# Kernel optimization log

Measured on AMD Instinct MI355X. Metric: run time of the kernel, lower is better.

The kernel has to match this reference:

```python
import jax, jax.numpy as jnp
import numpy as np

B, D, L, K = 262144, 64, 4, 8
BOUND = 3.0
MIN_BW = 1e-3   # min bin width
MIN_BH = 1e-3   # min bin height
MIN_D = 1e-3    # min derivative
MIN_LAM = 0.025 # min lambda
EPS = 1e-6


def _knots(lengths, lo, hi):
    # lengths: (D, K) normalized bin fractions -> (bin lengths (D,K), knot positions (D,K+1))
    knots = jnp.cumsum(lengths, axis=-1)
    knots = jnp.pad(knots, ((0, 0), (1, 0)))
    knots = (hi - lo) * knots + lo
    knots = knots.at[..., 0].set(lo)
    knots = knots.at[..., -1].set(hi)
    return knots[..., 1:] - knots[..., :-1], knots


def _gather(p, idx):
    # p: (D, K'), idx: (B, D) -> (B, D): per-dimension bin-parameter gather
    return p[jnp.arange(p.shape[0])[None, :], idx]


def spline_layer(x, uw, uh, ud, ul):
    # x: (B, D); uw/uh/ul: (D, K); ud: (D, K-1). Linear-order monotonic rational spline (pyro).
    w = jax.nn.softmax(uw, axis=-1)
    h = jax.nn.softmax(uh, axis=-1)
    d = jax.nn.softplus(ud)
    lam = jax.nn.sigmoid(ul)

    num_bins = w.shape[-1]
    left, right = -BOUND, BOUND
    inside = (x >= left) & (x <= right)
    xc = jnp.clip(x, left, right)  # identity applied outside; clamp keeps inside-branch math finite

    w = MIN_BW + (1.0 - MIN_BW * num_bins) * w
    h = MIN_BH + (1.0 - MIN_BH * num_bins) * h
    d = MIN_D + d
    widths, cumw = _knots(w, left, right)
    heights, cumh = _knots(h, left, right)
    d = jnp.pad(d, ((0, 0), (1, 1)), constant_values=1.0)  # boundary derivatives fixed to 1
    lam = (1.0 - 2.0 * MIN_LAM) * lam + MIN_LAM

    # data-dependent bin search (searchsorted via comparison-sum, as in pyro)
    bin_idx = jnp.sum(xc[..., None] >= (cumw + EPS)[None], axis=-1) - 1  # (B, D)
    bin_idx = jnp.clip(bin_idx, 0, num_bins - 1)

    iw = _gather(widths, bin_idx)
    icw = _gather(cumw, bin_idx)
    ich = _gather(cumh, bin_idx)
    idelta = _gather(heights / widths, bin_idx)
    id0 = _gather(d[:, :-1], bin_idx)
    id1 = _gather(d[:, 1:], bin_idx)
    ih = _gather(heights, bin_idx)
    il = _gather(lam, bin_idx)

    wa = 1.0
    wb = jnp.sqrt(id0 / id1) * wa
    wc = (il * wa * id0 + (1.0 - il) * wb * id1) / idelta
    ya = ich
    yb = ih + ich
    yc = ((1.0 - il) * wa * ya + il * wb * yb) / ((1.0 - il) * wa + il * wb)

    theta = (xc - icw) / iw
    lower = theta <= il
    num = jnp.where(lower, wa * ya * (il - theta) + wc * yc * theta,
                    wc * yc * (1.0 - theta) + wb * yb * (theta - il))
    den = jnp.where(lower, wa * (il - theta) + wc * theta,
                    wc * (1.0 - theta) + wb * (theta - il))
    out = num / den
    dnum = jnp.where(lower, wa * wc * il * (yc - ya), wb * wc * (1.0 - il) * (yb - yc)) / iw
    lad = jnp.log(dnum) - 2.0 * jnp.log(jnp.abs(den))

    out = jnp.where(inside, out, x)
    lad = jnp.where(inside, lad, 0.0)
    return out, jnp.sum(lad, axis=1)


def setup_inputs() -> dict:
    key = jax.random.key(0)
    k0, k1, k2, k3, k4 = jax.random.split(key, 5)
    return {
        "x": jax.random.normal(k0, (B, D), dtype=jnp.float32),
        "uw": jax.random.normal(k1, (L, D, K), dtype=jnp.float32),
        "uh": jax.random.normal(k2, (L, D, K), dtype=jnp.float32),
        "ud": jax.random.normal(k3, (L, D, K - 1), dtype=jnp.float32),
        "ul": jax.random.uniform(k4, (L, D, K), dtype=jnp.float32),
    }


def reference(x, uw, uh, ud, ul):
    def step(carry, params):
        xi, ld = carry
        pw, ph, pd, pl = params
        xi, l = spline_layer(xi, pw, ph, pd, pl)
        return (xi, ld + l), None
    init = (x, jnp.zeros(x.shape[0], x.dtype))
    (x, log_det), _ = jax.lax.scan(step, init, (uw, uh, ud, ul))
    return x, log_det
```

## Files before the change

kernel.cpp:

```cpp
#include <hip/hip_runtime.h>


#define BATCH 262144
#define DIM   64
#define NLAY  4
#define NK    8

#define OFF_KN0 0
#define OFF_KN1 2048
#define OFF_CRS 4096
#define OFF_CF0 4544

__global__ void nf_pre(const float* __restrict__ uw, const float* __restrict__ uh,
                       const float* __restrict__ ud, const float* __restrict__ ul,
                       float* __restrict__ F) {
  __shared__ double Lb[NLAY][17], Ly[NLAY][17], LM[NLAY][16][4], Ld[NLAY][16];
  __shared__ double sx[64], Fb[65];
  int d = blockIdx.x;
  int t = threadIdx.x;

  if (t < 32) {
    int l = t >> 3, k = t & 7;
    const float* pw  = uw + (l*DIM + d)*NK;
    const float* ph  = uh + (l*DIM + d)*NK;
    const float* pdv = ud + (l*DIM + d)*(NK-1);
    const float* pl  = ul + (l*DIM + d)*NK;

    float ev[NK];
    float mw = pw[0];
    for (int j = 1; j < NK; ++j) mw = fmaxf(mw, pw[j]);
    float sw = 0.f;
    for (int j = 0; j < NK; ++j) { ev[j] = expf(pw[j] - mw); sw += ev[j]; }
    float invw = 1.f / sw;
    float cwe = 0.f, cwi = 0.f;
    for (int j = 0; j <= k; ++j) {
      float vj = 1e-3f + (1.f - 1e-3f * (float)NK) * (ev[j] * invw);
      cwe = cwi; cwi += vj;
    }
    float kwL = (k == 0) ? -3.f : 6.f * cwe - 3.f;
    float kwR = (k == 7) ?  3.f : 6.f * cwi - 3.f;
    float wwk = kwR - kwL;

    float mh = ph[0];
    for (int j = 1; j < NK; ++j) mh = fmaxf(mh, ph[j]);
    float sh = 0.f;
    for (int j = 0; j < NK; ++j) { ev[j] = expf(ph[j] - mh); sh += ev[j]; }
    float invh = 1.f / sh;
    float che = 0.f, chi = 0.f;
    for (int j = 0; j <= k; ++j) {
      float vj = 1e-3f + (1.f - 1e-3f * (float)NK) * (ev[j] * invh);
      che = chi; chi += vj;
    }
    float khL = (k == 0) ? -3.f : 6.f * che - 3.f;
    float khR = (k == 7) ?  3.f : 6.f * chi - 3.f;
    float hhk = khR - khL;

    float dvk, dvk1;
    if (k == 0) dvk = 1.f;
    else { float u = pdv[k-1]; dvk  = 1e-3f + (fmaxf(u,0.f) + log1pf(expf(-fabsf(u)))); }
    if (k == 7) dvk1 = 1.f;
    else { float u = pdv[k];   dvk1 = 1e-3f + (fmaxf(u,0.f) + log1pf(expf(-fabsf(u)))); }
    float sg = 1.f / (1.f + expf(-pl[k]));
    float lmk = 0.95f * sg + 0.025f;

    float delta = hhk / wwk;
    float wbf = sqrtf(dvk / dvk1);
    float wcf = (lmk*dvk + (1.f-lmk)*wbf*dvk1) / delta;
    float yaf = khL, ybf = hhk + khL;
    float ycf = ((1.f-lmk)*yaf + lmk*wbf*ybf) / ((1.f-lmk) + lmk*wbf);

    if (k == 0) {
      Lb[l][0] = -3.0; Lb[l][16] = 3.0;
      Ly[l][0] = -3.0; Ly[l][16] = 3.0;
    }
    if (k) Lb[l][2*k] = (double)(kwL + 1.0e-6f);
    Lb[l][2*k+1] = (double)kwL + (double)lmk*(double)wwk;
    Ly[l][2*k]   = (double)yaf;
    Ly[l][2*k+1] = (double)ycf;

    double icw = (double)kwL, iw = (double)wwk, il = (double)lmk;
    double wb = wbf, wc = wcf, ya = yaf, yb = ybf, yc = ycf;
    double n0 = ya*il, n1 = wc*yc - ya, d0 = il, d1 = wc - 1.0;
    double A = n1, Bv = n0*iw - n1*icw, C = d1, Dv = d0*iw - d1*icw;
    LM[l][2*k][0]=A; LM[l][2*k][1]=Bv; LM[l][2*k][2]=C; LM[l][2*k][3]=Dv;
    Ld[l][2*k] = log2(A*Dv - Bv*C);
    n0 = wc*yc - il*wb*yb; n1 = wb*yb - wc*yc; d0 = wc - il*wb; d1 = wb - wc;
    A = n1; Bv = n0*iw - n1*icw; C = d1; Dv = d0*iw - d1*icw;
    LM[l][2*k+1][0]=A; LM[l][2*k+1][1]=Bv; LM[l][2*k+1][2]=C; LM[l][2*k+1][3]=Dv;
    Ld[l][2*k+1] = log2(A*Dv - Bv*C);
  }
  __syncthreads();

  if (t < 60) {
    int lp  = t / 15;
    int mth = t % 15 + 1;
    double x = Lb[lp][mth];
    for (int q = lp - 1; q >= 0; --q) {
      int j = 0;
      for (int k = 1; k <= 15; ++k) j += (x >= Ly[q][k]) ? 1 : 0;
      const double* M = LM[q][j];
      x = (M[3]*x - M[1]) / (M[0] - M[2]*x);
    }
    sx[t] = x;
  }
  __syncthreads();
  if (t < 60) {
    double x = sx[t];
    int r = 0;
    for (int s2 = 0; s2 < 60; ++s2) {
      double o = sx[s2];
      r += (o < x || (o == x && s2 < t)) ? 1 : 0;
    }
    Fb[r+1] = x;
  }
  if (t == 0)  Fb[0] = -3.0;
  if (t >= 60) Fb[t+1] = 3.0;
  __syncthreads();

  {
    int j = t;
    float bf;
    if (j == 0)       bf = -3.0f;
    else if (j <= 60) bf = (float)Fb[j];
    else              bf = 1e30f;
    int cw = j >> 3, r8 = j & 7;
    if (r8 < 4) F[OFF_KN0 + (cw*DIM + d)*4 + r8]     = bf;
    else        F[OFF_KN1 + (cw*DIM + d)*4 + (r8-4)] = bf;
    if (j >= 8 && (j & 7) == 0 && j <= 56) F[OFF_CRS + (j/8 - 1)*DIM + d] = bf;
  }

  if (t < 61) {
    int p = t;
    double bl = Fb[p], br = Fb[p+1];
    float xmf = (float)(0.5*(bl+br));
    xmf = fminf(fmaxf(xmf, -3.f), 3.f);
    double y = (double)xmf;
    double A=1.0, Bv=0.0, C=0.0, Dv=1.0, ld2 = 0.0;
    for (int q = 0; q < NLAY; ++q) {
      int j = 0;
      for (int k = 1; k <= 15; ++k) j += (y >= Lb[q][k]) ? 1 : 0;
      const double* M = LM[q][j];
      ld2 += Ld[q][j];
      double A2 = M[0]*A + M[1]*C, B2 = M[0]*Bv + M[1]*Dv;
      double C2 = M[2]*A + M[3]*C, D2 = M[2]*Bv + M[3]*Dv;
      y = (M[0]*y + M[1]) / (M[2]*y + M[3]);
      A=A2; Bv=B2; C=C2; Dv=D2;
    }
    double sinv = exp2(-0.5 * ld2);
    float4 c4;
    c4.x = (float)(A*sinv); c4.y = (float)(Bv*sinv);
    c4.z = (float)(C*sinv); c4.w = (float)(Dv*sinv);
    *(float4*)(F + OFF_CF0 + (size_t)(p*DIM + d)*4) = c4;
  }
}

template <int CTRL>
__device__ __forceinline__ float dpp_add(float x) {
  int yi = __builtin_amdgcn_update_dpp(0, __float_as_int(x), CTRL, 0xF, 0xF, false);
  return x + __int_as_float(yi);
}
__device__ __forceinline__ float wave_sum63(float x) {
  x = dpp_add<0x111>(x);
  x = dpp_add<0x112>(x);
  x = dpp_add<0x114>(x);
  x = dpp_add<0x118>(x);
  x = dpp_add<0x142>(x);
  x = dpp_add<0x143>(x);
  return x;
}

__global__ __launch_bounds__(1024, 4) void nf_main(const float* __restrict__ X,
                                                   const float* __restrict__ F,
                                                   float* __restrict__ OUT,
                                                   float* __restrict__ LDo) {
  __shared__ float smem[19712];
  int t = threadIdx.x;
  {
    float4* dst = (float4*)smem;
    const float4* kt = (const float4*)(F + OFF_KN0);
    dst[t] = kt[t];
    const float4* ct = (const float4*)(F + OFF_CF0);
    for (int i = t; i < 3904; i += 1024) dst[1024 + i] = ct[i];
  }
  int d = t & 63;
  float k1 = F[OFF_CRS + 0*DIM + d];
  float k2 = F[OFF_CRS + 1*DIM + d];
  float k3 = F[OFF_CRS + 2*DIM + d];
  float k4 = F[OFF_CRS + 3*DIM + d];
  float k5 = F[OFF_CRS + 4*DIM + d];
  float k6 = F[OFF_CRS + 5*DIM + d];
  float k7 = F[OFF_CRS + 6*DIM + d];
  __syncthreads();
  const float4* skv = (const float4*)smem;

  int gw = blockIdx.x * 16 + (t >> 6);
  const float* Xb = X   + (size_t)gw*32*DIM + d;
  float*       Ob = OUT + (size_t)gw*32*DIM + d;
  float*       Lp = LDo + (size_t)gw*32;

#define COARSE(xc) ((xc>=k1)+(xc>=k2)+(xc>=k3)+(xc>=k4)+(xc>=k5)+(xc>=k6)+(xc>=k7))
#define FINE(xc, cc, f0, f1) \
  ((cc<<3) + (int)(xc>=f0.y)+(int)(xc>=f0.z)+(int)(xc>=f0.w)+(int)(xc>=f1.x) \
           + (int)(xc>=f1.y)+(int)(xc>=f1.z)+(int)(xc>=f1.w))

  float xA0 = Xb[0],   xA1 = Xb[64];
  float xB0 = Xb[128], xB1 = Xb[192];
  float xC0 = Xb[256], xC1 = Xb[320];
  float xcA0 = fminf(fmaxf(xA0, -3.f), 3.f);
  float xcA1 = fminf(fmaxf(xA1, -3.f), 3.f);
  float4 cfA0, cfA1;
  {
    int c0 = COARSE(xcA0), c1 = COARSE(xcA1);
    float4 f00 = skv[(c0<<6)+d], f01 = skv[512+(c0<<6)+d];
    float4 f10 = skv[(c1<<6)+d], f11 = skv[512+(c1<<6)+d];
    int p0 = FINE(xcA0, c0, f00, f01);
    int p1 = FINE(xcA1, c1, f10, f11);
    cfA0 = skv[1024+(p0<<6)+d];
    cfA1 = skv[1024+(p1<<6)+d];
  }
  float xcB0 = fminf(fmaxf(xB0, -3.f), 3.f);
  float xcB1 = fminf(fmaxf(xB1, -3.f), 3.f);
  int cB0 = COARSE(xcB0), cB1 = COARSE(xcB1);
  float4 fB00 = skv[(cB0<<6)+d], fB01 = skv[512+(cB0<<6)+d];
  float4 fB10 = skv[(cB1<<6)+d], fB11 = skv[512+(cB1<<6)+d];

  for (int it = 0; it < 16; ++it) {
    float xcC0 = fminf(fmaxf(xC0, -3.f), 3.f);
    float xcC1 = fminf(fmaxf(xC1, -3.f), 3.f);
    int cC0 = COARSE(xcC0), cC1 = COARSE(xcC1);
    float4 fC00 = skv[(cC0<<6)+d], fC01 = skv[512+(cC0<<6)+d];
    float4 fC10 = skv[(cC1<<6)+d], fC11 = skv[512+(cC1<<6)+d];
    int u3 = (it + 3 < 16) ? (it + 3) : 15;
    float xN0 = Xb[u3*128], xN1 = Xb[u3*128 + 64];
    __builtin_amdgcn_sched_barrier(0);
    float num0 = fmaf(cfA0.x, xcA0, cfA0.y);
    float den0 = fmaf(cfA0.z, xcA0, cfA0.w);
    float o0 = (xA0 == xcA0) ? __fdividef(num0, den0) : xA0;
    float l0 = -1.3862943611198906f * __log2f(fabsf(den0));
    float num1 = fmaf(cfA1.x, xcA1, cfA1.y);
    float den1 = fmaf(cfA1.z, xcA1, cfA1.w);
    float o1 = (xA1 == xcA1) ? __fdividef(num1, den1) : xA1;
    float l1 = -1.3862943611198906f * __log2f(fabsf(den1));
    Ob[it*128] = o0; Ob[it*128 + 64] = o1;
    float s0 = wave_sum63(l0);
    float s1 = wave_sum63(l1);
    if (d == 63) {
      float2 v; v.x = s0; v.y = s1;
      *(float2*)(Lp + 2*it) = v;
    }
    __builtin_amdgcn_sched_barrier(0);
    int p0 = FINE(xcB0, cB0, fB00, fB01);
    int p1 = FINE(xcB1, cB1, fB10, fB11);
    float4 cfN0 = skv[1024+(p0<<6)+d];
    float4 cfN1 = skv[1024+(p1<<6)+d];
    xA0 = xB0; xA1 = xB1; xcA0 = xcB0; xcA1 = xcB1; cfA0 = cfN0; cfA1 = cfN1;
    xB0 = xC0; xB1 = xC1; xcB0 = xcC0; xcB1 = xcC1; cB0 = cC0; cB1 = cC1;
    fB00 = fC00; fB01 = fC01; fB10 = fC10; fB11 = fC11;
    xC0 = xN0; xC1 = xN1;
  }
#undef COARSE
#undef FINE
}

extern "C" void kernel_launch(void* const* d_in, const int* in_sizes, int n_in,
                              void* d_out, int out_size, void* d_ws, size_t ws_size,
                              hipStream_t stream) {
  const float* x  = (const float*)d_in[0];
  const float* uw = (const float*)d_in[1];
  const float* uh = (const float*)d_in[2];
  const float* ud = (const float*)d_in[3];
  const float* ul = (const float*)d_in[4];
  float* out = (float*)d_out;
  float* F = (float*)d_ws;
  nf_pre<<<DIM, 64, 0, stream>>>(uw, uh, ud, ul, F);
  nf_main<<<512, 1024, 0, stream>>>(x, F, out, out + (size_t)BATCH*DIM);
}
```

Baseline: 52.10 us.

## Vectorize main loop with float4 per lane and branchless binary bin search

```diff
diff --git a/kernel.cpp b/kernel.cpp
--- a/kernel.cpp
+++ b/kernel.cpp
@@ -9,7 +9,7 @@
 #define OFF_KN0 0
 #define OFF_KN1 2048
 #define OFF_CRS 4096
-#define OFF_CF0 4544
+#define OFF_CF  4544
 
 __global__ void nf_pre(const float* __restrict__ uw, const float* __restrict__ uh,
                        const float* __restrict__ ud, const float* __restrict__ ul,
@@ -117,149 +117,174 @@
   if (t >= 60) Fb[t+1] = 3.0;
   __syncthreads();
 
+  int pd = ((d >> 2) | ((d & 3) << 4));
+
   {
     int j = t;
     float bf;
     if (j == 0)       bf = -3.0f;
     else if (j <= 60) bf = (float)Fb[j];
+    else if (j == 61) bf = 3.0f;
     else              bf = 1e30f;
     int cw = j >> 3, r8 = j & 7;
-    if (r8 < 4) F[OFF_KN0 + (cw*DIM + d)*4 + r8]     = bf;
-    else        F[OFF_KN1 + (cw*DIM + d)*4 + (r8-4)] = bf;
-    if (j >= 8 && (j & 7) == 0 && j <= 56) F[OFF_CRS + (j/8 - 1)*DIM + d] = bf;
-  }
-
-  if (t < 61) {
-    int p = t;
-    double bl = Fb[p], br = Fb[p+1];
-    float xmf = (float)(0.5*(bl+br));
-    xmf = fminf(fmaxf(xmf, -3.f), 3.f);
-    double y = (double)xmf;
-    double A=1.0, Bv=0.0, C=0.0, Dv=1.0, ld2 = 0.0;
-    for (int q = 0; q < NLAY; ++q) {
-      int j = 0;
-      for (int k = 1; k <= 15; ++k) j += (y >= Lb[q][k]) ? 1 : 0;
-      const double* M = LM[q][j];
-      ld2 += Ld[q][j];
-      double A2 = M[0]*A + M[1]*C, B2 = M[0]*Bv + M[1]*Dv;
-      double C2 = M[2]*A + M[3]*C, D2 = M[2]*Bv + M[3]*Dv;
-      y = (M[0]*y + M[1]) / (M[2]*y + M[3]);
-      A=A2; Bv=B2; C=C2; Dv=D2;
-    }
-    double sinv = exp2(-0.5 * ld2);
+    if (r8 < 4) F[OFF_KN0 + (cw*DIM + pd)*4 + r8]     = bf;
+    else        F[OFF_KN1 + (cw*DIM + pd)*4 + (r8-4)] = bf;
+    if ((j & 7) == 7 && j <= 55) F[OFF_CRS + (j>>3)*DIM + d] = bf;
+  }
+
+  {
     float4 c4;
-    c4.x = (float)(A*sinv); c4.y = (float)(Bv*sinv);
-    c4.z = (float)(C*sinv); c4.w = (float)(Dv*sinv);
-    *(float4*)(F + OFF_CF0 + (size_t)(p*DIM + d)*4) = c4;
+    if (t == 0 || t >= 62) {
+      c4.x = 1.f; c4.y = 0.f; c4.z = 0.f; c4.w = 1.f;
+    } else {
+      int q = t - 1;
+      double bl = Fb[q], br = Fb[q+1];
+      float xmf = (float)(0.5*(bl+br));
+      xmf = fminf(fmaxf(xmf, -3.f), 3.f);
+      double y = (double)xmf;
+      double A=1.0, Bv=0.0, C=0.0, Dv=1.0, ld2 = 0.0;
+      for (int qq = 0; qq < NLAY; ++qq) {
+        int j = 0;
+        for (int k = 1; k <= 15; ++k) j += (y >= Lb[qq][k]) ? 1 : 0;
+        const double* M = LM[qq][j];
+        ld2 += Ld[qq][j];
+        double A2 = M[0]*A + M[1]*C, B2 = M[0]*Bv + M[1]*Dv;
+        double C2 = M[2]*A + M[3]*C, D2 = M[2]*Bv + M[3]*Dv;
+        y = (M[0]*y + M[1]) / (M[2]*y + M[3]);
+        A=A2; Bv=B2; C=C2; Dv=D2;
+      }
+      double sinv = exp2(-0.5 * ld2);
+      c4.x = (float)(A*sinv);  c4.y = (float)(Bv*sinv);
+      c4.z = (float)(C*sinv);  c4.w = (float)(Dv*sinv);
+    }
+    *(float4*)(F + OFF_CF + (size_t)(t*DIM + pd)*4) = c4;
   }
 }
 
 template <int CTRL>
 __device__ __forceinline__ float dpp_add(float x) {
-  int yi = __builtin_amdgcn_update_dpp(0, __float_as_int(x), CTRL, 0xF, 0xF, false);
+  int yi = __builtin_amdgcn_update_dpp(0, __float_as_int(x), CTRL, 0xF, 0xF, true);
   return x + __int_as_float(yi);
 }
-__device__ __forceinline__ float wave_sum63(float x) {
-  x = dpp_add<0x111>(x);
-  x = dpp_add<0x112>(x);
-  x = dpp_add<0x114>(x);
-  x = dpp_add<0x118>(x);
-  x = dpp_add<0x142>(x);
-  x = dpp_add<0x143>(x);
-  return x;
-}
+
+#define SRCH(xx, CR, COLB, CF)                                                 \
+  {                                                                            \
+    bool c2 = (xx) >= CR[3];                                                   \
+    float m5 = c2 ? CR[5] : CR[1];                                             \
+    bool c1 = (xx) >= m5;                                                      \
+    float m3 = c2 ? (c1 ? CR[6] : CR[4]) : (c1 ? CR[2] : CR[0]);               \
+    bool c0 = (xx) >= m3;                                                      \
+    int c = (((int)c2) << 2) | (((int)c1) << 1) | (int)c0;                     \
+    float4 f0 = kv[(c << 6) + COLB];                                           \
+    float4 f1 = kv[512 + (c << 6) + COLB];                                     \
+    bool b2 = (xx) >= f0.w;                                                    \
+    float n5 = b2 ? f1.y : f0.y;                                               \
+    bool b1 = (xx) >= n5;                                                      \
+    float n3 = b2 ? (b1 ? f1.z : f1.x) : (b1 ? f0.z : f0.x);                   \
+    bool b0 = (xx) >= n3;                                                      \
+    int p = (c << 3) | (((int)b2) << 2) | (((int)b1) << 1) | (int)b0;          \
+    CF = kv[1024 + (p << 6) + COLB];                                           \
+  }
+
+#define MTH(xx, CF, OO, LL)                                                    \
+  {                                                                            \
+    float nu = fmaf(CF.x, (xx), CF.y);                                         \
+    float de = fmaf(CF.z, (xx), CF.w);                                         \
+    OO = __fdividef(nu, de);                                                   \
+    LL = __log2f(fabsf(de));                                                   \
+  }
 
 __global__ __launch_bounds__(1024, 4) void nf_main(const float* __restrict__ X,
                                                    const float* __restrict__ F,
                                                    float* __restrict__ OUT,
                                                    float* __restrict__ LDo) {
-  __shared__ float smem[19712];
+  __shared__ float smem[20480];
   int t = threadIdx.x;
   {
     float4* dst = (float4*)smem;
-    const float4* kt = (const float4*)(F + OFF_KN0);
-    dst[t] = kt[t];
-    const float4* ct = (const float4*)(F + OFF_CF0);
-    for (int i = t; i < 3904; i += 1024) dst[1024 + i] = ct[i];
-  }
-  int d = t & 63;
-  float k1 = F[OFF_CRS + 0*DIM + d];
-  float k2 = F[OFF_CRS + 1*DIM + d];
-  float k3 = F[OFF_CRS + 2*DIM + d];
-  float k4 = F[OFF_CRS + 3*DIM + d];
-  float k5 = F[OFF_CRS + 4*DIM + d];
-  float k6 = F[OFF_CRS + 5*DIM + d];
-  float k7 = F[OFF_CRS + 6*DIM + d];
+    const float4* sk = (const float4*)F;
+    dst[t] = sk[t];
+    const float4* sc = (const float4*)(F + OFF_CF);
+#pragma unroll
+    for (int i = 0; i < 4; ++i) dst[1024 + t + i*1024] = sc[t + i*1024];
+  }
+  int lane = t & 63;
+  int m = lane & 15;
+  int rlane = lane >> 4;
+  float cr0[7], cr1[7], cr2[7], cr3[7];
+#pragma unroll
+  for (int k = 0; k < 7; ++k) {
+    cr0[k] = F[OFF_CRS + k*DIM + 4*m + 0];
+    cr1[k] = F[OFF_CRS + k*DIM + 4*m + 1];
+    cr2[k] = F[OFF_CRS + k*DIM + 4*m + 2];
+    cr3[k] = F[OFF_CRS + k*DIM + 4*m + 3];
+  }
   __syncthreads();
-  const float4* skv = (const float4*)smem;
+  const float4* kv = (const float4*)smem;
+  int col0 = m, col1 = m + 16, col2 = m + 32, col3 = m + 48;
 
   int gw = blockIdx.x * 16 + (t >> 6);
-  const float* Xb = X   + (size_t)gw*32*DIM + d;
-  float*       Ob = OUT + (size_t)gw*32*DIM + d;
-  float*       Lp = LDo + (size_t)gw*32;
-
-#define COARSE(xc) ((xc>=k1)+(xc>=k2)+(xc>=k3)+(xc>=k4)+(xc>=k5)+(xc>=k6)+(xc>=k7))
-#define FINE(xc, cc, f0, f1) \
-  ((cc<<3) + (int)(xc>=f0.y)+(int)(xc>=f0.z)+(int)(xc>=f0.w)+(int)(xc>=f1.x) \
-           + (int)(xc>=f1.y)+(int)(xc>=f1.z)+(int)(xc>=f1.w))
-
-  float xA0 = Xb[0],   xA1 = Xb[64];
-  float xB0 = Xb[128], xB1 = Xb[192];
-  float xC0 = Xb[256], xC1 = Xb[320];
-  float xcA0 = fminf(fmaxf(xA0, -3.f), 3.f);
-  float xcA1 = fminf(fmaxf(xA1, -3.f), 3.f);
-  float4 cfA0, cfA1;
+  const float4* Xq = (const float4*)(X + (size_t)gw*2048) + lane;
+  float4*       Oq = (float4*)(OUT + (size_t)gw*2048) + lane;
+  const float4* Pq = Xq + 128;
+  float*        Lps = LDo + (size_t)gw*32 + rlane;
+
+  float4 xA = Xq[0];
+  float4 cfA0, cfA1, cfA2, cfA3;
+  SRCH(xA.x, cr0, col0, cfA0)
+  SRCH(xA.y, cr1, col1, cfA1)
+  SRCH(xA.z, cr2, col2, cfA2)
+  SRCH(xA.w, cr3, col3, cfA3)
+  float4 xB = Xq[64];
+
+#define STEP(KS, PQOFF, BUMP)                                                  \
+  {                                                                            \
+    float4 xF = Pq[PQOFF];                                                     \
+    __builtin_amdgcn_sched_barrier(0);                                         \
+    float o0,o1,o2,o3,l0,l1,l2,l3;                                             \
+    MTH(xA.x, cfA0, o0, l0)                                                    \
+    MTH(xA.y, cfA1, o1, l1)                                                    \
+    MTH(xA.z, cfA2, o2, l2)                                                    \
+    MTH(xA.w, cfA3, o3, l3)                                                    \
+    float4 ov; ov.x=o0; ov.y=o1; ov.z=o2; ov.w=o3;                             \
+    Oq[(KS & 3) * 64] = ov;                                                    \
+    float s = (l0 + l1) + (l2 + l3);                                           \
+    s = dpp_add<0x111>(s); s = dpp_add<0x112>(s);                              \
+    s = dpp_add<0x114>(s); s = dpp_add<0x118>(s);                              \
+    s *= -1.3862943611198906f;                                                 \
+    if (m == 15) Lps[KS * 4] = s;                                              \
+    __builtin_amdgcn_sched_barrier(0);                                         \
+    SRCH(xB.x, cr0, col0, cfA0)                                                \
+    SRCH(xB.y, cr1, col1, cfA1)                                                \
+    SRCH(xB.z, cr2, col2, cfA2)                                                \
+    SRCH(xB.w, cr3, col3, cfA3)                                                \
+    xA = xB; xB = xF;                                                          \
+    if (BUMP) Pq += 64;                                                        \
+  }
+
+  STEP(0, 0, 1)
+  STEP(1, 0, 1)
+  STEP(2, 0, 1)
+  STEP(3, 0, 1)
+  Oq += 256;
+  STEP(4, 0, 1)
+  STEP(5, 0, 0)
+  STEP(6, 0, 0)
   {
-    int c0 = COARSE(xcA0), c1 = COARSE(xcA1);
-    float4 f00 = skv[(c0<<6)+d], f01 = skv[512+(c0<<6)+d];
-    float4 f10 = skv[(c1<<6)+d], f11 = skv[512+(c1<<6)+d];
-    int p0 = FINE(xcA0, c0, f00, f01);
-    int p1 = FINE(xcA1, c1, f10, f11);
-    cfA0 = skv[1024+(p0<<6)+d];
-    cfA1 = skv[1024+(p1<<6)+d];
-  }
-  float xcB0 = fminf(fmaxf(xB0, -3.f), 3.f);
-  float xcB1 = fminf(fmaxf(xB1, -3.f), 3.f);
-  int cB0 = COARSE(xcB0), cB1 = COARSE(xcB1);
-  float4 fB00 = skv[(cB0<<6)+d], fB01 = skv[512+(cB0<<6)+d];
-  float4 fB10 = skv[(cB1<<6)+d], fB11 = skv[512+(cB1<<6)+d];
-
-  for (int it = 0; it < 16; ++it) {
-    float xcC0 = fminf(fmaxf(xC0, -3.f), 3.f);
-    float xcC1 = fminf(fmaxf(xC1, -3.f), 3.f);
-    int cC0 = COARSE(xcC0), cC1 = COARSE(xcC1);
-    float4 fC00 = skv[(cC0<<6)+d], fC01 = skv[512+(cC0<<6)+d];
-    float4 fC10 = skv[(cC1<<6)+d], fC11 = skv[512+(cC1<<6)+d];
-    int u3 = (it + 3 < 16) ? (it + 3) : 15;
-    float xN0 = Xb[u3*128], xN1 = Xb[u3*128 + 64];
-    __builtin_amdgcn_sched_barrier(0);
-    float num0 = fmaf(cfA0.x, xcA0, cfA0.y);
-    float den0 = fmaf(cfA0.z, xcA0, cfA0.w);
-    float o0 = (xA0 == xcA0) ? __fdividef(num0, den0) : xA0;
-    float l0 = -1.3862943611198906f * __log2f(fabsf(den0));
-    float num1 = fmaf(cfA1.x, xcA1, cfA1.y);
-    float den1 = fmaf(cfA1.z, xcA1, cfA1.w);
-    float o1 = (xA1 == xcA1) ? __fdividef(num1, den1) : xA1;
-    float l1 = -1.3862943611198906f * __log2f(fabsf(den1));
-    Ob[it*128] = o0; Ob[it*128 + 64] = o1;
-    float s0 = wave_sum63(l0);
-    float s1 = wave_sum63(l1);
-    if (d == 63) {
-      float2 v; v.x = s0; v.y = s1;
-      *(float2*)(Lp + 2*it) = v;
-    }
-    __builtin_amdgcn_sched_barrier(0);
-    int p0 = FINE(xcB0, cB0, fB00, fB01);
-    int p1 = FINE(xcB1, cB1, fB10, fB11);
-    float4 cfN0 = skv[1024+(p0<<6)+d];
-    float4 cfN1 = skv[1024+(p1<<6)+d];
-    xA0 = xB0; xA1 = xB1; xcA0 = xcB0; xcA1 = xcB1; cfA0 = cfN0; cfA1 = cfN1;
-    xB0 = xC0; xB1 = xC1; xcB0 = xcC0; xcB1 = xcC1; cB0 = cC0; cB1 = cC1;
-    fB00 = fC00; fB01 = fC01; fB10 = fC10; fB11 = fC11;
-    xC0 = xN0; xC1 = xN1;
-  }
-#undef COARSE
-#undef FINE
+    float o0,o1,o2,o3,l0,l1,l2,l3;
+    MTH(xA.x, cfA0, o0, l0)
+    MTH(xA.y, cfA1, o1, l1)
+    MTH(xA.z, cfA2, o2, l2)
+    MTH(xA.w, cfA3, o3, l3)
+    float4 ov; ov.x=o0; ov.y=o1; ov.z=o2; ov.w=o3;
+    Oq[3 * 64] = ov;
+    float s = (l0 + l1) + (l2 + l3);
+    s = dpp_add<0x111>(s); s = dpp_add<0x112>(s);
+    s = dpp_add<0x114>(s); s = dpp_add<0x118>(s);
+    s *= -1.3862943611198906f;
+    if (m == 15) Lps[7 * 4] = s;
+  }
+#undef STEP
 }
 
 extern "C" void kernel_launch(void* const* d_in, const int* in_sizes, int n_in,
```

Measured after the change: 46.54 us. 10.7% less time.
